# Performance work log

Measured on AMD Instinct MI355X. Metric: run time of the kernel, lower is better.

The kernel has to match this reference:

```python
import jax, jax.numpy as jnp
import numpy as np

WS = 8          # window_size
NH = 6          # num_heads
C = 192         # in_channels
HD = C // NH    # head_dim
N = WS * WS     # tokens per window


def _relative_position_index(ws):
    coords = np.stack(np.meshgrid(np.arange(ws), np.arange(ws), indexing='ij'), axis=-1).reshape(-1, 2)
    rel = coords[:, None, :] - coords[None, :, :] + (ws - 1)  # [N,N,2] in [0, 2ws-2]
    return (rel[..., 0] * (2 * ws - 1) + rel[..., 1]).astype(np.int32)  # [N,N]


def setup_inputs() -> dict:
    key = jax.random.key(0)
    ks = jax.random.split(key, 10)
    s = 0.02
    B, H, W = 8, 128, 128
    inp = {
        'x': jax.random.normal(ks[0], (B, C, H, W), dtype=jnp.float32),
        'qkv_w': jax.random.normal(ks[1], (3 * C, C), dtype=jnp.float32) * s,
        'qkv_b': jnp.zeros((3 * C,), dtype=jnp.float32),
        'proj_w': jax.random.normal(ks[2], (C, C), dtype=jnp.float32) * s,
        'proj_b': jnp.zeros((C,), dtype=jnp.float32),
        'mlp1_w': jax.random.normal(ks[3], (2 * C, C), dtype=jnp.float32) * s,
        'mlp1_b': jnp.zeros((2 * C,), dtype=jnp.float32),
        'mlp2_w': jax.random.normal(ks[4], (C, C), dtype=jnp.float32) * s,
        'mlp2_b': jnp.zeros((C,), dtype=jnp.float32),
        'bias_table': jax.random.normal(ks[5], ((2 * WS - 1) ** 2,), dtype=jnp.float32) * s,
        'rel_index': jnp.asarray(_relative_position_index(WS)),
    }
    return inp


def reference(x, qkv_w, qkv_b, proj_w, proj_b, mlp1_w, mlp1_b, mlp2_w, mlp2_b, bias_table, rel_index):
    B, _, H, W = x.shape
    nwh, nww = H // WS, W // WS
    # ---- window partition: [B,C,H,W] -> [B*nWin, N, C]
    xw = x.reshape(B, C, nwh, WS, nww, WS).transpose(0, 2, 4, 3, 5, 1).reshape(-1, N, C)
    # ---- qkv projection
    qkv = xw @ qkv_w.T + qkv_b  # [Bn, N, 3C]
    q, k, v = jnp.split(qkv, 3, axis=-1)
    split_heads = lambda t: t.reshape(-1, N, NH, HD).transpose(0, 2, 1, 3)  # [Bn,NH,N,HD]
    q, k, v = split_heads(q), split_heads(k), split_heads(v)
    # ---- learned relative-position bias (WindowScoreBias), broadcast over batch & heads
    bias = bias_table[rel_index]  # [N,N]
    scores = jnp.einsum('bhnd,bhmd->bhnm', q, k) * (1.0 / jnp.sqrt(jnp.float32(HD))) + bias
    attn = jax.nn.softmax(scores, axis=-1)
    out = jnp.einsum('bhnm,bhmd->bhnd', attn, v)  # [Bn,NH,N,HD]
    out = out.transpose(0, 2, 1, 3).reshape(-1, N, C)
    out = out @ proj_w.T + proj_b
    # ---- window merge back to BCHW
    out = out.reshape(B, nwh, nww, WS, WS, C).transpose(0, 5, 1, 3, 2, 4).reshape(B, C, H, W)
    x = x + out  # residual 1
    # ---- pointwise GLU MLP (1x1 convs as channel einsums)
    h = jnp.einsum('bchw,oc->bohw', x, mlp1_w) + mlp1_b[None, :, None, None]
    a, b = jnp.split(h, 2, axis=1)
    g = a * jax.nn.sigmoid(b)
    m = jnp.einsum('bchw,oc->bohw', g, mlp2_w) + mlp2_b[None, :, None, None]
    return x + m  # residual 2
```

## Files before the change

### kernel.cpp

```cpp
#include <hip/hip_runtime.h>


typedef short          s16x8 __attribute__((ext_vector_type(8)));
typedef unsigned short u16x4 __attribute__((ext_vector_type(4)));
typedef unsigned short u16x8 __attribute__((ext_vector_type(8)));
typedef float          f32x4 __attribute__((ext_vector_type(4)));

#define MFMA(A, B, C) __builtin_amdgcn_mfma_f32_16x16x32_bf16((A), (B), (C), 0, 0, 0)

__device__ __forceinline__ unsigned short f2b(float f) {
  unsigned x = __float_as_uint(f);
  x = (x + 0x7FFFu + ((x >> 16) & 1u)) >> 16;
  return (unsigned short)x;
}
__device__ __forceinline__ float b2f(unsigned short u) {
  return __uint_as_float(((unsigned)u) << 16);
}

__device__ __forceinline__ int swz32(int t, int c) {
  return t * 32 + ((((c >> 3) ^ (t >> 1)) & 3) << 3) + (c & 7);
}
__device__ __forceinline__ int swzV(int d, int t) {
  return d * 64 + ((((t >> 3) ^ (d + (d >> 3))) & 7) << 3) + (t & 7);
}

#define XSTR   200
__device__ __forceinline__ int xsw(int t, int c) {
  return t * XSTR + ((((c >> 3) ^ ((t >> 3) & 7))) << 3) + (c & 7);
}

#define WSLOT  37376
#define QSCALE 0.17677669529663687f

#define WOFF_QKV   0
#define WOFF_PROJ  110592
#define WOFF_MLP1  147456
#define WOFF_MLP2  221184
#define WOFF_BIASX_BYTES 516096
#define WOFF_YWIN_BYTES  532480

__global__ void prep_kernel(const float* __restrict__ qkv_w,
                            const float* __restrict__ proj_w,
                            const float* __restrict__ mlp1_w,
                            const float* __restrict__ mlp2_w,
                            const float* __restrict__ bias_table,
                            const int*   __restrict__ rel_index,
                            unsigned short* __restrict__ qkv_wb,
                            unsigned short* __restrict__ proj_wb,
                            unsigned short* __restrict__ mlp1_wb,
                            unsigned short* __restrict__ mlp2_wb,
                            float* __restrict__ biasx) {
  int j = blockIdx.x * 256 + threadIdx.x;
  if (j < 110592) {
    float v = qkv_w[j];
    if (j < 36864) v *= QSCALE;
    qkv_wb[j] = f2b(v);
  } else if (j < 147456) {
    proj_wb[j - 110592] = f2b(proj_w[j - 110592]);
  } else if (j < 221184) {
    mlp1_wb[j - 147456] = f2b(mlp1_w[j - 147456]);
  } else if (j < 258048) {
    mlp2_wb[j - 221184] = f2b(mlp2_w[j - 221184]);
  } else {
    int e = j - 258048;
    int l = e >> 6, v = e & 63;
    int tm = v >> 4, tn = (v >> 2) & 3, r = v & 3;
    int q = tn * 16 + (l & 15);
    int k = tm * 16 + (l >> 4) * 4 + r;
    biasx[e] = bias_table[rel_index[q * 64 + k]];
  }
}

__global__ __launch_bounds__(768, 3) void attn_kernel(
    const float* __restrict__ x,
    const unsigned short* __restrict__ qkv_wb, const float* __restrict__ qkv_b,
    const unsigned short* __restrict__ proj_wb, const float* __restrict__ proj_b,
    const float* __restrict__ biasx,
    unsigned short* __restrict__ y_win) {
  __shared__ __align__(16) unsigned short sm[2 * WSLOT];

  const int tid  = threadIdx.x;
  const int lane = tid & 63;
  const int wv   = tid >> 6;
  const int wid  = (wv >= 6) ? 1 : 0;
  const int hd   = wv - wid * 6;
  const int l15  = lane & 15;
  const int lg   = lane >> 4;
  const int pair = ((blockIdx.x & 7) << 7) | (blockIdx.x >> 3);
  const int wins0 = pair * 2;

  const float* xwb[2];
#pragma unroll
  for (int wi = 0; wi < 2; ++wi) {
    const int w = wins0 + wi;
    xwb[wi] = x + (size_t)(w >> 8) * 192 * 16384
                + (size_t)(((w >> 4) & 15) * 8) * 128 + (w & 15) * 8;
  }

#pragma unroll
  for (int it = 0; it < 4; ++it) {
    int job = tid + 768 * it;
    int wi = job / 1536;
    int j = job - wi * 1536;
    int c = j >> 3, i = j & 7;
    const float* src = xwb[wi] + (size_t)c * 16384 + i * 128;
    f32x4 v0 = *(const f32x4*)(src);
    f32x4 v1 = *(const f32x4*)(src + 4);
    unsigned short* dst = &sm[wi * WSLOT + (((c >> 3) ^ i) << 3) + (c & 7)];
    dst[(i * 8 + 0) * XSTR] = f2b(v0[0]); dst[(i * 8 + 1) * XSTR] = f2b(v0[1]);
    dst[(i * 8 + 2) * XSTR] = f2b(v0[2]); dst[(i * 8 + 3) * XSTR] = f2b(v0[3]);
    dst[(i * 8 + 4) * XSTR] = f2b(v1[0]); dst[(i * 8 + 5) * XSTR] = f2b(v1[1]);
    dst[(i * 8 + 6) * XSTR] = f2b(v1[2]); dst[(i * 8 + 7) * XSTR] = f2b(v1[3]);
  }
  __syncthreads();

  unsigned short* xa = sm + wid * WSLOT;
  unsigned short* hb = xa + 12800 + hd * 4096;
  unsigned short* R0 = hb;
  unsigned short* R1 = hb + 2048;
  const int oQ = hd * 32;

  f32x4 accqT[2][4], acckT[2][4], accv[4][2];
#pragma unroll
  for (int m = 0; m < 2; ++m) {
    f32x4 bq4 = *(const f32x4*)&qkv_b[oQ + m * 16 + lg * 4];
    f32x4 bk4 = *(const f32x4*)&qkv_b[192 + oQ + m * 16 + lg * 4];
#pragma unroll
    for (int tn = 0; tn < 4; ++tn) {
      accqT[m][tn] = bq4 * QSCALE;
      acckT[m][tn] = bk4;
    }
  }
#pragma unroll
  for (int nt = 0; nt < 2; ++nt) {
    const float bv = qkv_b[384 + oQ + nt * 16 + l15];
#pragma unroll
    for (int mt = 0; mt < 4; ++mt) accv[mt][nt] = (f32x4){bv, bv, bv, bv};
  }
#pragma unroll
  for (int ks = 0; ks < 6; ++ks) {
    const int k0 = ks * 32 + lg * 8;
    s16x8 bf[4];
#pragma unroll
    for (int tn = 0; tn < 4; ++tn)
      bf[tn] = *(const s16x8*)&xa[xsw(tn * 16 + l15, k0)];
    s16x8 wq[2], wk[2], wvv[2];
#pragma unroll
    for (int m = 0; m < 2; ++m) {
      wq[m] = *(const s16x8*)&qkv_wb[(size_t)(oQ + m * 16 + l15) * 192 + k0];
      wk[m] = *(const s16x8*)&qkv_wb[(size_t)(192 + oQ + m * 16 + l15) * 192 + k0];
      wvv[m] = *(const s16x8*)&qkv_wb[(size_t)(384 + oQ + m * 16 + l15) * 192 + k0];
    }
#pragma unroll
    for (int m = 0; m < 2; ++m)
#pragma unroll
      for (int tn = 0; tn < 4; ++tn) {
        accqT[m][tn] = MFMA(wq[m], bf[tn], accqT[m][tn]);
        acckT[m][tn] = MFMA(wk[m], bf[tn], acckT[m][tn]);
      }
#pragma unroll
    for (int mt = 0; mt < 4; ++mt)
#pragma unroll
      for (int nt = 0; nt < 2; ++nt)
        accv[mt][nt] = MFMA(bf[mt], wvv[nt], accv[mt][nt]);
  }
#pragma unroll
  for (int m = 0; m < 2; ++m)
#pragma unroll
    for (int tn = 0; tn < 4; ++tn) {
      const int t = tn * 16 + l15, d0 = m * 16 + lg * 4;
      u16x4 q4, k4;
#pragma unroll
      for (int r = 0; r < 4; ++r) {
        q4[r] = f2b(accqT[m][tn][r]);
        k4[r] = f2b(acckT[m][tn][r]);
      }
      *(u16x4*)&R0[swz32(t, d0)] = q4;
      *(u16x4*)&R1[swz32(t, d0)] = k4;
    }
  u16x4 vreg[4][2];
#pragma unroll
  for (int mt = 0; mt < 4; ++mt)
#pragma unroll
    for (int nt = 0; nt < 2; ++nt) {
      vreg[mt][nt][0] = f2b(accv[mt][nt][0]); vreg[mt][nt][1] = f2b(accv[mt][nt][1]);
      vreg[mt][nt][2] = f2b(accv[mt][nt][2]); vreg[mt][nt][3] = f2b(accv[mt][nt][3]);
    }

  const float* bxp = biasx + lane * 64;
  s16x8 kf[4], qf[4];
#pragma unroll
  for (int tm = 0; tm < 4; ++tm)
    kf[tm] = *(const s16x8*)&R1[swz32(tm * 16 + l15, lg * 8)];
#pragma unroll
  for (int tn = 0; tn < 4; ++tn)
    qf[tn] = *(const s16x8*)&R0[swz32(tn * 16 + l15, lg * 8)];
#pragma unroll
  for (int mt = 0; mt < 4; ++mt)
#pragma unroll
    for (int nt = 0; nt < 2; ++nt)
      *(u16x4*)&R1[swzV(nt * 16 + l15, mt * 16 + lg * 4)] = vreg[mt][nt];

  f32x4 sc[4][4];
#pragma unroll
  for (int tm = 0; tm < 4; ++tm)
#pragma unroll
    for (int tn = 0; tn < 4; ++tn) {
      f32x4 bfr = *(const f32x4*)&bxp[tm * 16 + tn * 4];
      sc[tm][tn] = MFMA(kf[tm], qf[tn], bfr);
    }
#pragma unroll
  for (int tn = 0; tn < 4; ++tn) {
    float mx = sc[0][tn][0];
#pragma unroll
    for (int tm = 0; tm < 4; ++tm)
#pragma unroll
      for (int r = 0; r < 4; ++r) mx = fmaxf(mx, sc[tm][tn][r]);
    mx = fmaxf(mx, __shfl_xor(mx, 16));
    mx = fmaxf(mx, __shfl_xor(mx, 32));
    float sum = 0.f;
#pragma unroll
    for (int tm = 0; tm < 4; ++tm)
#pragma unroll
      for (int r = 0; r < 4; ++r) {
        float e = __expf(sc[tm][tn][r] - mx);
        sc[tm][tn][r] = e;
        sum += e;
      }
    sum += __shfl_xor(sum, 16);
    sum += __shfl_xor(sum, 32);
    const float inv = 1.0f / sum;
#pragma unroll
    for (int tm = 0; tm < 4; ++tm)
#pragma unroll
      for (int r = 0; r < 4; ++r) sc[tm][tn][r] *= inv;
  }

  f32x4 oT[2][4];
#pragma unroll
  for (int m = 0; m < 2; ++m)
#pragma unroll
    for (int tn = 0; tn < 4; ++tn) oT[m][tn] = (f32x4){0.f, 0.f, 0.f, 0.f};
#pragma unroll
  for (int half = 0; half < 2; ++half) {
#pragma unroll
    for (int tm = 0; tm < 2; ++tm)
#pragma unroll
      for (int tn = 0; tn < 4; ++tn) {
        u16x4 p4;
#pragma unroll
        for (int r = 0; r < 4; ++r) p4[r] = f2b(sc[half * 2 + tm][tn][r]);
        *(u16x4*)&R0[swz32(tn * 16 + l15, tm * 16 + lg * 4)] = p4;
      }
    s16x8 bp[4], av[2];
#pragma unroll
    for (int tn = 0; tn < 4; ++tn)
      bp[tn] = *(const s16x8*)&R0[swz32(tn * 16 + l15, lg * 8)];
#pragma unroll
    for (int m = 0; m < 2; ++m)
      av[m] = *(const s16x8*)&R1[swzV(m * 16 + l15, half * 32 + lg * 8)];
#pragma unroll
    for (int m = 0; m < 2; ++m)
#pragma unroll
      for (int tn = 0; tn < 4; ++tn)
        oT[m][tn] = MFMA(av[m], bp[tn], oT[m][tn]);
  }
#pragma unroll
  for (int m = 0; m < 2; ++m)
#pragma unroll
    for (int tn = 0; tn < 4; ++tn) {
      u16x4 a4;
#pragma unroll
      for (int r = 0; r < 4; ++r) a4[r] = f2b(oT[m][tn][r]);
      *(u16x4*)&R0[swz32(tn * 16 + l15, m * 16 + lg * 4)] = a4;
    }
  __syncthreads();

  f32x4 pjT[2][4];
#pragma unroll
  for (int m = 0; m < 2; ++m) {
    f32x4 bp4 = *(const f32x4*)&proj_b[oQ + m * 16 + lg * 4];
#pragma unroll
    for (int tn = 0; tn < 4; ++tn) pjT[m][tn] = bp4;
  }
#pragma unroll
  for (int hh = 0; hh < 6; ++hh) {
    const unsigned short* aoh = xa + 12800 + hh * 4096;
    s16x8 aa[4];
#pragma unroll
    for (int tn = 0; tn < 4; ++tn)
      aa[tn] = *(const s16x8*)&aoh[swz32(tn * 16 + l15, lg * 8)];
    s16x8 wp[2];
#pragma unroll
    for (int m = 0; m < 2; ++m)
      wp[m] = *(const s16x8*)&proj_wb[(size_t)(oQ + m * 16 + l15) * 192 + hh * 32 + lg * 8];
#pragma unroll
    for (int m = 0; m < 2; ++m)
#pragma unroll
      for (int tn = 0; tn < 4; ++tn)
        pjT[m][tn] = MFMA(wp[m], aa[tn], pjT[m][tn]);
  }
#pragma unroll
  for (int m = 0; m < 2; ++m)
#pragma unroll
    for (int tn = 0; tn < 4; ++tn) {
      const int t = tn * 16 + l15, o0 = oQ + m * 16 + lg * 4;
      const int ad = xsw(t, o0);
      u16x4 old = *(const u16x4*)&xa[ad];
      u16x4 nw;
#pragma unroll
      for (int r = 0; r < 4; ++r) nw[r] = f2b(pjT[m][tn][r] + b2f(old[r]));
      *(u16x4*)&xa[ad] = nw;
    }
  __syncthreads();
#pragma unroll
  for (int it = 0; it < 4; ++it) {
    int job = tid + 768 * it;
    int wi = job / 1536;
    int j = job - wi * 1536;
    int t = j / 24;
    int seg = j - t * 24;
    unsigned short* ywp = y_win + (size_t)(wins0 + wi) * 12288;
    *(u16x8*)&ywp[(size_t)j * 8] = *(const u16x8*)&sm[wi * WSLOT + xsw(t, seg * 8)];
  }
}

__global__ __launch_bounds__(256, 4) void mlp_kernel(
    const unsigned short* __restrict__ y_win,
    const unsigned short* __restrict__ w1b, const float* __restrict__ b1,
    const unsigned short* __restrict__ w2b, const float* __restrict__ b2,
    float* __restrict__ out) {
  __shared__ __align__(16) unsigned short sm2[2 * 64 * XSTR];
  unsigned short* yb = sm2;
  unsigned short* wk = sm2 + 64 * XSTR;

  const int tid  = threadIdx.x;
  const int lane = tid & 63;
  const int wv   = tid >> 6;
  const int l15  = lane & 15;
  const int lg   = lane >> 4;
  const int win  = ((blockIdx.x & 7) << 8) | (blockIdx.x >> 3);
  const int bb   = win >> 8;
  const int wh   = (win >> 4) & 15;
  const int wwi  = win & 15;

  const unsigned short* ywp = y_win + (size_t)win * 12288;
#pragma unroll
  for (int it = 0; it < 6; ++it) {
    int job = tid + 256 * it;
    int t = job / 24;
    int seg = job - t * 24;
    *(u16x8*)&yb[t * XSTR + seg * 8] = *(const u16x8*)&ywp[(size_t)job * 8];
  }
  __syncthreads();

#pragma unroll
  for (int i = 0; i < 3; ++i) {
    const int na = (3 * wv + i) * 16 + l15;
    const int nb = na + 192;
    f32x4 aacc[4], bacc[4];
    const float ba = b1[na], bbv = b1[nb];
#pragma unroll
    for (int m = 0; m < 4; ++m) {
      aacc[m] = (f32x4){ba, ba, ba, ba};
      bacc[m] = (f32x4){bbv, bbv, bbv, bbv};
    }
#pragma unroll
    for (int ks = 0; ks < 6; ++ks) {
      const int k0 = ks * 32 + lg * 8;
      s16x8 af[4];
#pragma unroll
      for (int m = 0; m < 4; ++m)
        af[m] = *(const s16x8*)&yb[(m * 16 + l15) * XSTR + k0];
      s16x8 wa = *(const s16x8*)&w1b[(size_t)na * 192 + k0];
      s16x8 wb = *(const s16x8*)&w1b[(size_t)nb * 192 + k0];
#pragma unroll
      for (int m = 0; m < 4; ++m) {
        aacc[m] = MFMA(af[m], wa, aacc[m]);
        bacc[m] = MFMA(af[m], wb, bacc[m]);
      }
    }
#pragma unroll
    for (int m = 0; m < 4; ++m)
#pragma unroll
      for (int r = 0; r < 4; ++r) {
        const float g = aacc[m][r] * (1.0f / (1.0f + __expf(-bacc[m][r])));
        wk[(m * 16 + lg * 4 + r) * XSTR + na] = f2b(g);
      }
  }
  __syncthreads();

  int ocol[3];
  f32x4 macc[4][3];
#pragma unroll
  for (int i = 0; i < 3; ++i) {
    ocol[i] = (3 * wv + i) * 16 + l15;
    const float bb2 = b2[ocol[i]];
#pragma unroll
    for (int m = 0; m < 4; ++m) macc[m][i] = (f32x4){bb2, bb2, bb2, bb2};
  }
#pragma unroll
  for (int ks = 0; ks < 6; ++ks) {
    const int k0 = ks * 32 + lg * 8;
    s16x8 gf[4];
#pragma unroll
    for (int m = 0; m < 4; ++m)
      gf[m] = *(const s16x8*)&wk[(m * 16 + l15) * XSTR + k0];
#pragma unroll
    for (int i = 0; i < 3; ++i) {
      s16x8 wf = *(const s16x8*)&w2b[(size_t)ocol[i] * 192 + k0];
#pragma unroll
      for (int m = 0; m < 4; ++m) macc[m][i] = MFMA(gf[m], wf, macc[m][i]);
    }
  }
  __syncthreads();
#pragma unroll
  for (int m = 0; m < 4; ++m)
#pragma unroll
    for (int i = 0; i < 3; ++i)
#pragma unroll
      for (int r = 0; r < 4; ++r)
        wk[(m * 16 + lg * 4 + r) * XSTR + ocol[i]] = f2b(macc[m][i][r]);
  __syncthreads();

  float* obase = out + (size_t)bb * 192 * 16384 + (size_t)(wh * 8) * 128 + wwi * 8;
#pragma unroll
  for (int it = 0; it < 6; ++it) {
    int job = tid + 256 * it;
    int i = job / 192;
    int c = job - i * 192;
    float vals[8];
#pragma unroll
    for (int j = 0; j < 8; ++j) {
      const int t = i * 8 + j;
      vals[j] = b2f(yb[t * XSTR + c]) + b2f(wk[t * XSTR + c]);
    }
    float* dst = obase + (size_t)c * 16384 + i * 128;
    f32x4 o0 = {vals[0], vals[1], vals[2], vals[3]};
    f32x4 o1 = {vals[4], vals[5], vals[6], vals[7]};
    *(f32x4*)dst = o0;
    *(f32x4*)(dst + 4) = o1;
  }
}

extern "C" void kernel_launch(void* const* d_in, const int* in_sizes, int n_in,
                              void* d_out, int out_size, void* d_ws, size_t ws_size,
                              hipStream_t stream) {
  (void)in_sizes; (void)n_in; (void)out_size; (void)ws_size;
  const float* x          = (const float*)d_in[0];
  const float* qkv_w      = (const float*)d_in[1];
  const float* qkv_b      = (const float*)d_in[2];
  const float* proj_w     = (const float*)d_in[3];
  const float* proj_b     = (const float*)d_in[4];
  const float* mlp1_w     = (const float*)d_in[5];
  const float* mlp1_b     = (const float*)d_in[6];
  const float* mlp2_w     = (const float*)d_in[7];
  const float* mlp2_b     = (const float*)d_in[8];
  const float* bias_table = (const float*)d_in[9];
  const int*   rel_index  = (const int*)d_in[10];
  float* out = (float*)d_out;

  char* ws = (char*)d_ws;
  unsigned short* qkv_wb  = (unsigned short*)ws + WOFF_QKV;
  unsigned short* proj_wb = (unsigned short*)ws + WOFF_PROJ;
  unsigned short* mlp1_wb = (unsigned short*)ws + WOFF_MLP1;
  unsigned short* mlp2_wb = (unsigned short*)ws + WOFF_MLP2;
  float*          biasx   = (float*)(ws + WOFF_BIASX_BYTES);
  unsigned short* y_win   = (unsigned short*)(ws + WOFF_YWIN_BYTES);

  hipLaunchKernelGGL(prep_kernel, dim3(1024), dim3(256), 0, stream,
                     qkv_w, proj_w, mlp1_w, mlp2_w, bias_table, rel_index,
                     qkv_wb, proj_wb, mlp1_wb, mlp2_wb, biasx);
  hipLaunchKernelGGL(attn_kernel, dim3(1024), dim3(768), 0, stream,
                     x, qkv_wb, qkv_b, proj_wb, proj_b, biasx, y_win);
  hipLaunchKernelGGL(mlp_kernel, dim3(2048), dim3(256), 0, stream,
                     y_win, mlp1_wb, mlp1_b, mlp2_wb, mlp2_b, out);
}
```

Before: 236.1 us.

## Fuse GLU MLP into attention kernel, eliminating y_win global round-trip

```diff
diff --git a/kernel.cpp b/kernel.cpp
--- a/kernel.cpp
+++ b/kernel.cpp
@@ -15,6 +15,11 @@
 }
 __device__ __forceinline__ float b2f(unsigned short u) {
   return __uint_as_float(((unsigned)u) << 16);
+}
+__device__ __forceinline__ u16x4 pk4(f32x4 v) {
+  u16x4 r;
+  r[0] = f2b(v[0]); r[1] = f2b(v[1]); r[2] = f2b(v[2]); r[3] = f2b(v[3]);
+  return r;
 }
 
 __device__ __forceinline__ int swz32(int t, int c) {
@@ -37,7 +42,6 @@
 #define WOFF_MLP1  147456
 #define WOFF_MLP2  221184
 #define WOFF_BIASX_BYTES 516096
-#define WOFF_YWIN_BYTES  532480
 
 __global__ void prep_kernel(const float* __restrict__ qkv_w,
                             const float* __restrict__ proj_w,
@@ -71,12 +75,14 @@
   }
 }
 
-__global__ __launch_bounds__(768, 3) void attn_kernel(
+__global__ __launch_bounds__(768, 3) void fused_kernel(
     const float* __restrict__ x,
     const unsigned short* __restrict__ qkv_wb, const float* __restrict__ qkv_b,
     const unsigned short* __restrict__ proj_wb, const float* __restrict__ proj_b,
     const float* __restrict__ biasx,
-    unsigned short* __restrict__ y_win) {
+    const unsigned short* __restrict__ w1b, const float* __restrict__ b1,
+    const unsigned short* __restrict__ w2b, const float* __restrict__ b2,
+    float* __restrict__ out) {
   __shared__ __align__(16) unsigned short sm[2 * WSLOT];
 
   const int tid  = threadIdx.x;
@@ -90,11 +96,14 @@
   const int wins0 = pair * 2;
 
   const float* xwb[2];
+  float* owb[2];
 #pragma unroll
   for (int wi = 0; wi < 2; ++wi) {
     const int w = wins0 + wi;
-    xwb[wi] = x + (size_t)(w >> 8) * 192 * 16384
-                + (size_t)(((w >> 4) & 15) * 8) * 128 + (w & 15) * 8;
+    const size_t off = (size_t)(w >> 8) * 192 * 16384
+                     + (size_t)(((w >> 4) & 15) * 8) * 128 + (w & 15) * 8;
+    xwb[wi] = x + off;
+    owb[wi] = out + off;
   }
 
 #pragma unroll
@@ -169,23 +178,15 @@
 #pragma unroll
     for (int tn = 0; tn < 4; ++tn) {
       const int t = tn * 16 + l15, d0 = m * 16 + lg * 4;
-      u16x4 q4, k4;
-#pragma unroll
-      for (int r = 0; r < 4; ++r) {
-        q4[r] = f2b(accqT[m][tn][r]);
-        k4[r] = f2b(acckT[m][tn][r]);
-      }
-      *(u16x4*)&R0[swz32(t, d0)] = q4;
-      *(u16x4*)&R1[swz32(t, d0)] = k4;
+      *(u16x4*)&R0[swz32(t, d0)] = pk4(accqT[m][tn]);
+      *(u16x4*)&R1[swz32(t, d0)] = pk4(acckT[m][tn]);
     }
   u16x4 vreg[4][2];
 #pragma unroll
   for (int mt = 0; mt < 4; ++mt)
 #pragma unroll
-    for (int nt = 0; nt < 2; ++nt) {
-      vreg[mt][nt][0] = f2b(accv[mt][nt][0]); vreg[mt][nt][1] = f2b(accv[mt][nt][1]);
-      vreg[mt][nt][2] = f2b(accv[mt][nt][2]); vreg[mt][nt][3] = f2b(accv[mt][nt][3]);
-    }
+    for (int nt = 0; nt < 2; ++nt)
+      vreg[mt][nt] = pk4(accv[mt][nt]);
 
   const float* bxp = biasx + lane * 64;
   s16x8 kf[4], qf[4];
@@ -246,12 +247,9 @@
 #pragma unroll
     for (int tm = 0; tm < 2; ++tm)
 #pragma unroll
-      for (int tn = 0; tn < 4; ++tn) {
-        u16x4 p4;
-#pragma unroll
-        for (int r = 0; r < 4; ++r) p4[r] = f2b(sc[half * 2 + tm][tn][r]);
-        *(u16x4*)&R0[swz32(tn * 16 + l15, tm * 16 + lg * 4)] = p4;
-      }
+      for (int tn = 0; tn < 4; ++tn)
+        *(u16x4*)&R0[swz32(tn * 16 + l15, tm * 16 + lg * 4)] =
+            pk4(sc[half * 2 + tm][tn]);
     s16x8 bp[4], av[2];
 #pragma unroll
     for (int tn = 0; tn < 4; ++tn)
@@ -268,12 +266,8 @@
 #pragma unroll
   for (int m = 0; m < 2; ++m)
 #pragma unroll
-    for (int tn = 0; tn < 4; ++tn) {
-      u16x4 a4;
-#pragma unroll
-      for (int r = 0; r < 4; ++r) a4[r] = f2b(oT[m][tn][r]);
-      *(u16x4*)&R0[swz32(tn * 16 + l15, m * 16 + lg * 4)] = a4;
-    }
+    for (int tn = 0; tn < 4; ++tn)
+      *(u16x4*)&R0[swz32(tn * 16 + l15, m * 16 + lg * 4)] = pk4(oT[m][tn]);
   __syncthreads();
 
   f32x4 pjT[2][4];
@@ -307,135 +301,116 @@
       const int t = tn * 16 + l15, o0 = oQ + m * 16 + lg * 4;
       const int ad = xsw(t, o0);
       u16x4 old = *(const u16x4*)&xa[ad];
-      u16x4 nw;
-#pragma unroll
-      for (int r = 0; r < 4; ++r) nw[r] = f2b(pjT[m][tn][r] + b2f(old[r]));
-      *(u16x4*)&xa[ad] = nw;
-    }
-  __syncthreads();
+      f32x4 s;
+#pragma unroll
+      for (int r = 0; r < 4; ++r) s[r] = pjT[m][tn][r] + b2f(old[r]);
+      *(u16x4*)&xa[ad] = pk4(s);
+    }
+  __syncthreads();
+
+  unsigned short* gb = xa + 12800;
+
+  {
+    f32x4 accA[2][4], accB[2][4];
+#pragma unroll
+    for (int ma = 0; ma < 2; ++ma) {
+      f32x4 ba4 = *(const f32x4*)&b1[oQ + ma * 16 + lg * 4];
+      f32x4 bb4 = *(const f32x4*)&b1[192 + oQ + ma * 16 + lg * 4];
+#pragma unroll
+      for (int tn = 0; tn < 4; ++tn) {
+        accA[ma][tn] = ba4;
+        accB[ma][tn] = bb4;
+      }
+    }
+#pragma unroll
+    for (int ks = 0; ks < 6; ++ks) {
+      const int k0 = ks * 32 + lg * 8;
+      s16x8 bf[4];
+#pragma unroll
+      for (int tn = 0; tn < 4; ++tn)
+        bf[tn] = *(const s16x8*)&xa[xsw(tn * 16 + l15, k0)];
+      s16x8 wa[2], wb[2];
+#pragma unroll
+      for (int ma = 0; ma < 2; ++ma) {
+        wa[ma] = *(const s16x8*)&w1b[(size_t)(oQ + ma * 16 + l15) * 192 + k0];
+        wb[ma] = *(const s16x8*)&w1b[(size_t)(192 + oQ + ma * 16 + l15) * 192 + k0];
+      }
+#pragma unroll
+      for (int ma = 0; ma < 2; ++ma)
+#pragma unroll
+        for (int tn = 0; tn < 4; ++tn) {
+          accA[ma][tn] = MFMA(wa[ma], bf[tn], accA[ma][tn]);
+          accB[ma][tn] = MFMA(wb[ma], bf[tn], accB[ma][tn]);
+        }
+    }
+#pragma unroll
+    for (int ma = 0; ma < 2; ++ma)
+#pragma unroll
+      for (int tn = 0; tn < 4; ++tn) {
+        const int t = tn * 16 + l15, c0 = oQ + ma * 16 + lg * 4;
+        f32x4 gv;
+#pragma unroll
+        for (int r = 0; r < 4; ++r) {
+          const float a = accA[ma][tn][r];
+          const float bgl = accB[ma][tn][r];
+          gv[r] = a * (1.0f / (1.0f + __expf(-bgl)));
+        }
+        *(u16x4*)&gb[xsw(t, c0)] = pk4(gv);
+      }
+  }
+  __syncthreads();
+
+  f32x4 macc[2][4];
+#pragma unroll
+  for (int mo = 0; mo < 2; ++mo) {
+    f32x4 b24 = *(const f32x4*)&b2[oQ + mo * 16 + lg * 4];
+#pragma unroll
+    for (int tn = 0; tn < 4; ++tn) macc[mo][tn] = b24;
+  }
+#pragma unroll
+  for (int ks = 0; ks < 6; ++ks) {
+    const int k0 = ks * 32 + lg * 8;
+    s16x8 gf[4];
+#pragma unroll
+    for (int tn = 0; tn < 4; ++tn)
+      gf[tn] = *(const s16x8*)&gb[xsw(tn * 16 + l15, k0)];
+    s16x8 ww[2];
+#pragma unroll
+    for (int mo = 0; mo < 2; ++mo)
+      ww[mo] = *(const s16x8*)&w2b[(size_t)(oQ + mo * 16 + l15) * 192 + k0];
+#pragma unroll
+    for (int mo = 0; mo < 2; ++mo)
+#pragma unroll
+      for (int tn = 0; tn < 4; ++tn)
+        macc[mo][tn] = MFMA(ww[mo], gf[tn], macc[mo][tn]);
+  }
+  __syncthreads();
+#pragma unroll
+  for (int mo = 0; mo < 2; ++mo)
+#pragma unroll
+    for (int tn = 0; tn < 4; ++tn) {
+      const int t = tn * 16 + l15, c0 = oQ + mo * 16 + lg * 4;
+      *(u16x4*)&gb[xsw(t, c0)] = pk4(macc[mo][tn]);
+    }
+  __syncthreads();
+
 #pragma unroll
   for (int it = 0; it < 4; ++it) {
     int job = tid + 768 * it;
     int wi = job / 1536;
     int j = job - wi * 1536;
-    int t = j / 24;
-    int seg = j - t * 24;
-    unsigned short* ywp = y_win + (size_t)(wins0 + wi) * 12288;
-    *(u16x8*)&ywp[(size_t)j * 8] = *(const u16x8*)&sm[wi * WSLOT + xsw(t, seg * 8)];
-  }
-}
-
-__global__ __launch_bounds__(256, 4) void mlp_kernel(
-    const unsigned short* __restrict__ y_win,
-    const unsigned short* __restrict__ w1b, const float* __restrict__ b1,
-    const unsigned short* __restrict__ w2b, const float* __restrict__ b2,
-    float* __restrict__ out) {
-  __shared__ __align__(16) unsigned short sm2[2 * 64 * XSTR];
-  unsigned short* yb = sm2;
-  unsigned short* wk = sm2 + 64 * XSTR;
-
-  const int tid  = threadIdx.x;
-  const int lane = tid & 63;
-  const int wv   = tid >> 6;
-  const int l15  = lane & 15;
-  const int lg   = lane >> 4;
-  const int win  = ((blockIdx.x & 7) << 8) | (blockIdx.x >> 3);
-  const int bb   = win >> 8;
-  const int wh   = (win >> 4) & 15;
-  const int wwi  = win & 15;
-
-  const unsigned short* ywp = y_win + (size_t)win * 12288;
-#pragma unroll
-  for (int it = 0; it < 6; ++it) {
-    int job = tid + 256 * it;
-    int t = job / 24;
-    int seg = job - t * 24;
-    *(u16x8*)&yb[t * XSTR + seg * 8] = *(const u16x8*)&ywp[(size_t)job * 8];
-  }
-  __syncthreads();
-
-#pragma unroll
-  for (int i = 0; i < 3; ++i) {
-    const int na = (3 * wv + i) * 16 + l15;
-    const int nb = na + 192;
-    f32x4 aacc[4], bacc[4];
-    const float ba = b1[na], bbv = b1[nb];
-#pragma unroll
-    for (int m = 0; m < 4; ++m) {
-      aacc[m] = (f32x4){ba, ba, ba, ba};
-      bacc[m] = (f32x4){bbv, bbv, bbv, bbv};
-    }
-#pragma unroll
-    for (int ks = 0; ks < 6; ++ks) {
-      const int k0 = ks * 32 + lg * 8;
-      s16x8 af[4];
-#pragma unroll
-      for (int m = 0; m < 4; ++m)
-        af[m] = *(const s16x8*)&yb[(m * 16 + l15) * XSTR + k0];
-      s16x8 wa = *(const s16x8*)&w1b[(size_t)na * 192 + k0];
-      s16x8 wb = *(const s16x8*)&w1b[(size_t)nb * 192 + k0];
-#pragma unroll
-      for (int m = 0; m < 4; ++m) {
-        aacc[m] = MFMA(af[m], wa, aacc[m]);
-        bacc[m] = MFMA(af[m], wb, bacc[m]);
-      }
-    }
-#pragma unroll
-    for (int m = 0; m < 4; ++m)
-#pragma unroll
-      for (int r = 0; r < 4; ++r) {
-        const float g = aacc[m][r] * (1.0f / (1.0f + __expf(-bacc[m][r])));
-        wk[(m * 16 + lg * 4 + r) * XSTR + na] = f2b(g);
-      }
-  }
-  __syncthreads();
-
-  int ocol[3];
-  f32x4 macc[4][3];
-#pragma unroll
-  for (int i = 0; i < 3; ++i) {
-    ocol[i] = (3 * wv + i) * 16 + l15;
-    const float bb2 = b2[ocol[i]];
-#pragma unroll
-    for (int m = 0; m < 4; ++m) macc[m][i] = (f32x4){bb2, bb2, bb2, bb2};
-  }
-#pragma unroll
-  for (int ks = 0; ks < 6; ++ks) {
-    const int k0 = ks * 32 + lg * 8;
-    s16x8 gf[4];
-#pragma unroll
-    for (int m = 0; m < 4; ++m)
-      gf[m] = *(const s16x8*)&wk[(m * 16 + l15) * XSTR + k0];
-#pragma unroll
-    for (int i = 0; i < 3; ++i) {
-      s16x8 wf = *(const s16x8*)&w2b[(size_t)ocol[i] * 192 + k0];
-#pragma unroll
-      for (int m = 0; m < 4; ++m) macc[m][i] = MFMA(gf[m], wf, macc[m][i]);
-    }
-  }
-  __syncthreads();
-#pragma unroll
-  for (int m = 0; m < 4; ++m)
-#pragma unroll
-    for (int i = 0; i < 3; ++i)
-#pragma unroll
-      for (int r = 0; r < 4; ++r)
-        wk[(m * 16 + lg * 4 + r) * XSTR + ocol[i]] = f2b(macc[m][i][r]);
-  __syncthreads();
-
-  float* obase = out + (size_t)bb * 192 * 16384 + (size_t)(wh * 8) * 128 + wwi * 8;
-#pragma unroll
-  for (int it = 0; it < 6; ++it) {
-    int job = tid + 256 * it;
-    int i = job / 192;
-    int c = job - i * 192;
+    int i = j / 192;
+    int c = j - i * 192;
+    const unsigned short* yb = sm + wi * WSLOT;
+    const unsigned short* mb = yb + 12800;
     float vals[8];
 #pragma unroll
-    for (int j = 0; j < 8; ++j) {
-      const int t = i * 8 + j;
-      vals[j] = b2f(yb[t * XSTR + c]) + b2f(wk[t * XSTR + c]);
-    }
-    float* dst = obase + (size_t)c * 16384 + i * 128;
+    for (int jj = 0; jj < 8; ++jj) {
+      const int t = i * 8 + jj;
+      const int ad = xsw(t, c);
+      vals[jj] = b2f(yb[ad]) + b2f(mb[ad]);
+    }
+    float* dst = owb[wi] + (size_t)c * 16384 + i * 128;
     f32x4 o0 = {vals[0], vals[1], vals[2], vals[3]};
     f32x4 o1 = {vals[4], vals[5], vals[6], vals[7]};
     *(f32x4*)dst = o0;
@@ -466,13 +441,11 @@
   unsigned short* mlp1_wb = (unsigned short*)ws + WOFF_MLP1;
   unsigned short* mlp2_wb = (unsigned short*)ws + WOFF_MLP2;
   float*          biasx   = (float*)(ws + WOFF_BIASX_BYTES);
-  unsigned short* y_win   = (unsigned short*)(ws + WOFF_YWIN_BYTES);
 
   hipLaunchKernelGGL(prep_kernel, dim3(1024), dim3(256), 0, stream,
                      qkv_w, proj_w, mlp1_w, mlp2_w, bias_table, rel_index,
                      qkv_wb, proj_wb, mlp1_wb, mlp2_wb, biasx);
-  hipLaunchKernelGGL(attn_kernel, dim3(1024), dim3(768), 0, stream,
-                     x, qkv_wb, qkv_b, proj_wb, proj_b, biasx, y_win);
-  hipLaunchKernelGGL(mlp_kernel, dim3(2048), dim3(256), 0, stream,
-                     y_win, mlp1_wb, mlp1_b, mlp2_wb, mlp2_b, out);
-}
+  hipLaunchKernelGGL(fused_kernel, dim3(1024), dim3(768), 0, stream,
+                     x, qkv_wb, qkv_b, proj_wb, proj_b, biasx,
+                     mlp1_wb, mlp1_b, mlp2_wb, mlp2_b, out);
+}
```

Result: slower. 249.6 us (+5.7%).

## Split window partition into separate transpose kernel and shrink attention LDS

Applied to the files above, without the earlier changes.

```diff
diff --git a/kernel.cpp b/kernel.cpp
--- a/kernel.cpp
+++ b/kernel.cpp
@@ -16,6 +16,11 @@
 __device__ __forceinline__ float b2f(unsigned short u) {
   return __uint_as_float(((unsigned)u) << 16);
 }
+__device__ __forceinline__ u16x4 pk4(f32x4 v) {
+  u16x4 r;
+  r[0] = f2b(v[0]); r[1] = f2b(v[1]); r[2] = f2b(v[2]); r[3] = f2b(v[3]);
+  return r;
+}
 
 __device__ __forceinline__ int swz32(int t, int c) {
   return t * 32 + ((((c >> 3) ^ (t >> 1)) & 3) << 3) + (c & 7);
@@ -25,11 +30,6 @@
 }
 
 #define XSTR   200
-__device__ __forceinline__ int xsw(int t, int c) {
-  return t * XSTR + ((((c >> 3) ^ ((t >> 3) & 7))) << 3) + (c & 7);
-}
-
-#define WSLOT  37376
 #define QSCALE 0.17677669529663687f
 
 #define WOFF_QKV   0
@@ -37,7 +37,7 @@
 #define WOFF_MLP1  147456
 #define WOFF_MLP2  221184
 #define WOFF_BIASX_BYTES 516096
-#define WOFF_YWIN_BYTES  532480
+#define WOFF_XW_BYTES    532480
 
 __global__ void prep_kernel(const float* __restrict__ qkv_w,
                             const float* __restrict__ proj_w,
@@ -71,13 +71,55 @@
   }
 }
 
+#define TSTR 129
+__global__ __launch_bounds__(256) void xpose_kernel(
+    const float* __restrict__ x, unsigned short* __restrict__ xw) {
+  __shared__ unsigned short tb[192 * TSTR];
+  const int tid = threadIdx.x;
+  const int s   = ((blockIdx.x & 7) << 7) | (blockIdx.x >> 3);
+  const int b   = s >> 7;
+  const int hr  = s & 127;
+  const float* xrow = x + (size_t)b * 192 * 16384 + (size_t)hr * 128;
+
+#pragma unroll
+  for (int it = 0; it < 3; ++it) {
+    int job = tid + 256 * it;
+    int c = job >> 2, wseg = job & 3;
+    const float* src = xrow + (size_t)c * 16384 + wseg * 32;
+    unsigned short* dst = &tb[c * TSTR + wseg * 32];
+#pragma unroll
+    for (int q = 0; q < 8; ++q) {
+      f32x4 v = *(const f32x4*)(src + q * 4);
+      u16x4 p; p[0] = f2b(v[0]); p[1] = f2b(v[1]); p[2] = f2b(v[2]); p[3] = f2b(v[3]);
+      *(u16x4*)&dst[q * 4] = p;
+    }
+  }
+  __syncthreads();
+
+  const int winb = b * 256 + (hr >> 3) * 16;
+  const int i = hr & 7;
+#pragma unroll
+  for (int it = 0; it < 12; ++it) {
+    int job = tid + 256 * it;
+    int wwi = job / 192;
+    int rem = job - wwi * 192;
+    int t7 = rem / 24;
+    int cseg = rem - t7 * 24;
+    u16x8 v;
+#pragma unroll
+    for (int jj = 0; jj < 8; ++jj)
+      v[jj] = tb[(cseg * 8 + jj) * TSTR + wwi * 8 + t7];
+    unsigned short* dst = xw + (size_t)(winb + wwi) * 12288 + (i * 8 + t7) * 192 + cseg * 8;
+    *(u16x8*)dst = v;
+  }
+}
+
 __global__ __launch_bounds__(768, 3) void attn_kernel(
-    const float* __restrict__ x,
+    const unsigned short* __restrict__ xw,
     const unsigned short* __restrict__ qkv_wb, const float* __restrict__ qkv_b,
     const unsigned short* __restrict__ proj_wb, const float* __restrict__ proj_b,
-    const float* __restrict__ biasx,
-    unsigned short* __restrict__ y_win) {
-  __shared__ __align__(16) unsigned short sm[2 * WSLOT];
+    const float* __restrict__ biasx) {
+  __shared__ __align__(16) unsigned short sm[2 * 6 * 4096];
 
   const int tid  = threadIdx.x;
   const int lane = tid & 63;
@@ -87,38 +129,13 @@
   const int l15  = lane & 15;
   const int lg   = lane >> 4;
   const int pair = ((blockIdx.x & 7) << 7) | (blockIdx.x >> 3);
-  const int wins0 = pair * 2;
-
-  const float* xwb[2];
-#pragma unroll
-  for (int wi = 0; wi < 2; ++wi) {
-    const int w = wins0 + wi;
-    xwb[wi] = x + (size_t)(w >> 8) * 192 * 16384
-                + (size_t)(((w >> 4) & 15) * 8) * 128 + (w & 15) * 8;
-  }
-
-#pragma unroll
-  for (int it = 0; it < 4; ++it) {
-    int job = tid + 768 * it;
-    int wi = job / 1536;
-    int j = job - wi * 1536;
-    int c = j >> 3, i = j & 7;
-    const float* src = xwb[wi] + (size_t)c * 16384 + i * 128;
-    f32x4 v0 = *(const f32x4*)(src);
-    f32x4 v1 = *(const f32x4*)(src + 4);
-    unsigned short* dst = &sm[wi * WSLOT + (((c >> 3) ^ i) << 3) + (c & 7)];
-    dst[(i * 8 + 0) * XSTR] = f2b(v0[0]); dst[(i * 8 + 1) * XSTR] = f2b(v0[1]);
-    dst[(i * 8 + 2) * XSTR] = f2b(v0[2]); dst[(i * 8 + 3) * XSTR] = f2b(v0[3]);
-    dst[(i * 8 + 4) * XSTR] = f2b(v1[0]); dst[(i * 8 + 5) * XSTR] = f2b(v1[1]);
-    dst[(i * 8 + 6) * XSTR] = f2b(v1[2]); dst[(i * 8 + 7) * XSTR] = f2b(v1[3]);
-  }
-  __syncthreads();
-
-  unsigned short* xa = sm + wid * WSLOT;
-  unsigned short* hb = xa + 12800 + hd * 4096;
-  unsigned short* R0 = hb;
-  unsigned short* R1 = hb + 2048;
-  const int oQ = hd * 32;
+  const int win  = pair * 2 + wid;
+  const int oQ   = hd * 32;
+
+  unsigned short* xww = (unsigned short*)xw + (size_t)win * 12288;
+  unsigned short* hb  = sm + (wid * 6 + hd) * 4096;
+  unsigned short* R0  = hb;
+  unsigned short* R1  = hb + 2048;
 
   f32x4 accqT[2][4], acckT[2][4], accv[4][2];
 #pragma unroll
@@ -143,12 +160,12 @@
     s16x8 bf[4];
 #pragma unroll
     for (int tn = 0; tn < 4; ++tn)
-      bf[tn] = *(const s16x8*)&xa[xsw(tn * 16 + l15, k0)];
+      bf[tn] = *(const s16x8*)&xww[(tn * 16 + l15) * 192 + k0];
     s16x8 wq[2], wk[2], wvv[2];
 #pragma unroll
     for (int m = 0; m < 2; ++m) {
-      wq[m] = *(const s16x8*)&qkv_wb[(size_t)(oQ + m * 16 + l15) * 192 + k0];
-      wk[m] = *(const s16x8*)&qkv_wb[(size_t)(192 + oQ + m * 16 + l15) * 192 + k0];
+      wq[m]  = *(const s16x8*)&qkv_wb[(size_t)(oQ + m * 16 + l15) * 192 + k0];
+      wk[m]  = *(const s16x8*)&qkv_wb[(size_t)(192 + oQ + m * 16 + l15) * 192 + k0];
       wvv[m] = *(const s16x8*)&qkv_wb[(size_t)(384 + oQ + m * 16 + l15) * 192 + k0];
     }
 #pragma unroll
@@ -169,23 +186,15 @@
 #pragma unroll
     for (int tn = 0; tn < 4; ++tn) {
       const int t = tn * 16 + l15, d0 = m * 16 + lg * 4;
-      u16x4 q4, k4;
-#pragma unroll
-      for (int r = 0; r < 4; ++r) {
-        q4[r] = f2b(accqT[m][tn][r]);
-        k4[r] = f2b(acckT[m][tn][r]);
-      }
-      *(u16x4*)&R0[swz32(t, d0)] = q4;
-      *(u16x4*)&R1[swz32(t, d0)] = k4;
+      *(u16x4*)&R0[swz32(t, d0)] = pk4(accqT[m][tn]);
+      *(u16x4*)&R1[swz32(t, d0)] = pk4(acckT[m][tn]);
     }
   u16x4 vreg[4][2];
 #pragma unroll
   for (int mt = 0; mt < 4; ++mt)
 #pragma unroll
-    for (int nt = 0; nt < 2; ++nt) {
-      vreg[mt][nt][0] = f2b(accv[mt][nt][0]); vreg[mt][nt][1] = f2b(accv[mt][nt][1]);
-      vreg[mt][nt][2] = f2b(accv[mt][nt][2]); vreg[mt][nt][3] = f2b(accv[mt][nt][3]);
-    }
+    for (int nt = 0; nt < 2; ++nt)
+      vreg[mt][nt] = pk4(accv[mt][nt]);
 
   const float* bxp = biasx + lane * 64;
   s16x8 kf[4], qf[4];
@@ -246,12 +255,9 @@
 #pragma unroll
     for (int tm = 0; tm < 2; ++tm)
 #pragma unroll
-      for (int tn = 0; tn < 4; ++tn) {
-        u16x4 p4;
-#pragma unroll
-        for (int r = 0; r < 4; ++r) p4[r] = f2b(sc[half * 2 + tm][tn][r]);
-        *(u16x4*)&R0[swz32(tn * 16 + l15, tm * 16 + lg * 4)] = p4;
-      }
+      for (int tn = 0; tn < 4; ++tn)
+        *(u16x4*)&R0[swz32(tn * 16 + l15, tm * 16 + lg * 4)] =
+            pk4(sc[half * 2 + tm][tn]);
     s16x8 bp[4], av[2];
 #pragma unroll
     for (int tn = 0; tn < 4; ++tn)
@@ -268,12 +274,8 @@
 #pragma unroll
   for (int m = 0; m < 2; ++m)
 #pragma unroll
-    for (int tn = 0; tn < 4; ++tn) {
-      u16x4 a4;
-#pragma unroll
-      for (int r = 0; r < 4; ++r) a4[r] = f2b(oT[m][tn][r]);
-      *(u16x4*)&R0[swz32(tn * 16 + l15, m * 16 + lg * 4)] = a4;
-    }
+    for (int tn = 0; tn < 4; ++tn)
+      *(u16x4*)&R0[swz32(tn * 16 + l15, m * 16 + lg * 4)] = pk4(oT[m][tn]);
   __syncthreads();
 
   f32x4 pjT[2][4];
@@ -285,7 +287,7 @@
   }
 #pragma unroll
   for (int hh = 0; hh < 6; ++hh) {
-    const unsigned short* aoh = xa + 12800 + hh * 4096;
+    const unsigned short* aoh = sm + (wid * 6 + hh) * 4096;
     s16x8 aa[4];
 #pragma unroll
     for (int tn = 0; tn < 4; ++tn)
@@ -305,24 +307,12 @@
 #pragma unroll
     for (int tn = 0; tn < 4; ++tn) {
       const int t = tn * 16 + l15, o0 = oQ + m * 16 + lg * 4;
-      const int ad = xsw(t, o0);
-      u16x4 old = *(const u16x4*)&xa[ad];
-      u16x4 nw;
-#pragma unroll
-      for (int r = 0; r < 4; ++r) nw[r] = f2b(pjT[m][tn][r] + b2f(old[r]));
-      *(u16x4*)&xa[ad] = nw;
-    }
-  __syncthreads();
-#pragma unroll
-  for (int it = 0; it < 4; ++it) {
-    int job = tid + 768 * it;
-    int wi = job / 1536;
-    int j = job - wi * 1536;
-    int t = j / 24;
-    int seg = j - t * 24;
-    unsigned short* ywp = y_win + (size_t)(wins0 + wi) * 12288;
-    *(u16x8*)&ywp[(size_t)j * 8] = *(const u16x8*)&sm[wi * WSLOT + xsw(t, seg * 8)];
-  }
+      u16x4 old = *(const u16x4*)&xww[t * 192 + o0];
+      f32x4 s;
+#pragma unroll
+      for (int r = 0; r < 4; ++r) s[r] = pjT[m][tn][r] + b2f(old[r]);
+      *(u16x4*)&xww[t * 192 + o0] = pk4(s);
+    }
 }
 
 __global__ __launch_bounds__(256, 4) void mlp_kernel(
@@ -466,13 +456,14 @@
   unsigned short* mlp1_wb = (unsigned short*)ws + WOFF_MLP1;
   unsigned short* mlp2_wb = (unsigned short*)ws + WOFF_MLP2;
   float*          biasx   = (float*)(ws + WOFF_BIASX_BYTES);
-  unsigned short* y_win   = (unsigned short*)(ws + WOFF_YWIN_BYTES);
+  unsigned short* xw      = (unsigned short*)(ws + WOFF_XW_BYTES);
 
   hipLaunchKernelGGL(prep_kernel, dim3(1024), dim3(256), 0, stream,
                      qkv_w, proj_w, mlp1_w, mlp2_w, bias_table, rel_index,
                      qkv_wb, proj_wb, mlp1_wb, mlp2_wb, biasx);
+  hipLaunchKernelGGL(xpose_kernel, dim3(1024), dim3(256), 0, stream, x, xw);
   hipLaunchKernelGGL(attn_kernel, dim3(1024), dim3(768), 0, stream,
-                     x, qkv_wb, qkv_b, proj_wb, proj_b, biasx, y_win);
+                     xw, qkv_wb, qkv_b, proj_wb, proj_b, biasx);
   hipLaunchKernelGGL(mlp_kernel, dim3(2048), dim3(256), 0, stream,
-                     y_win, mlp1_wb, mlp1_b, mlp2_wb, mlp2_b, out);
-}
+                     xw, mlp1_wb, mlp1_b, mlp2_wb, mlp2_b, out);
+}
```

Result: slower. 321.0 us (+36.0%).
